# Kernel optimization log

Measured on AMD Instinct MI355X. Metric: run time of the kernel, lower is better.

## Reference

```python
import jax, jax.numpy as jnp
import numpy as np

N_NODES = 100000
N_EDGES = 1600000
IN_FEATS = 128
HIDDEN = 64
OUT_FEATS = 64
N_LABELS = 8


def setup_inputs() -> dict:
    key = jax.random.key(0)
    ks = jax.random.split(key, 10)
    glorot = lambda k, fi, fo: jax.random.normal(k, (fi, fo), jnp.float32) * jnp.sqrt(2.0 / (fi + fo))
    return {
        "features": jax.random.normal(ks[0], (N_NODES, IN_FEATS), jnp.float32),
        "edge_src": jax.random.randint(ks[1], (N_EDGES,), 0, N_NODES, jnp.int32),
        "edge_dst": jax.random.randint(ks[2], (N_EDGES,), 0, N_NODES, jnp.int32),
        "edge_types": jax.random.randint(ks[3], (N_EDGES,), 0, 4, jnp.int32),
        "W1": glorot(ks[4], IN_FEATS, HIDDEN),
        "b1": jnp.zeros((HIDDEN,), jnp.float32),
        "W2": glorot(ks[5], HIDDEN, OUT_FEATS),
        "b2": jnp.zeros((OUT_FEATS,), jnp.float32),
        "Wp": glorot(ks[6], OUT_FEATS, N_LABELS),
        "bp": jnp.zeros((N_LABELS,), jnp.float32),
    }


def _degree_norms(edge_src, edge_dst, n_nodes):
    ones = jnp.ones(edge_src.shape[0], jnp.float32)
    deg_out = jax.ops.segment_sum(ones, edge_src, num_segments=n_nodes)
    deg_in = jax.ops.segment_sum(ones, edge_dst, num_segments=n_nodes)
    # DGL clamps degrees to min 1 before pow(-0.5)
    norm_src = jnp.maximum(deg_out, 1.0) ** -0.5  # [N]
    norm_dst = jnp.maximum(deg_in, 1.0) ** -0.5   # [N]
    return norm_src, norm_dst


def _graph_conv(x, W, b, edge_src, edge_dst, norm_src, norm_dst, n_nodes):
    # norm='both': scale src, dense transform first (mult_first), aggregate, scale dst
    h = (x * norm_src[:, None]) @ W            # [N, out]
    msg = h[edge_src]                          # [E, out] gather
    agg = jax.ops.segment_sum(msg, edge_dst, num_segments=n_nodes)  # [N, out] scatter-add
    return agg * norm_dst[:, None] + b


def reference(features, edge_src, edge_dst, edge_types, W1, b1, W2, b2, Wp, bp):
    n_nodes = features.shape[0]
    norm_src, norm_dst = _degree_norms(edge_src, edge_dst, n_nodes)
    x = jax.nn.relu(_graph_conv(features, W1, b1, edge_src, edge_dst, norm_src, norm_dst, n_nodes))
    # dropout is identity in eval mode
    x = jax.nn.relu(_graph_conv(x, W2, b2, edge_src, edge_dst, norm_src, norm_dst, n_nodes))
    logits = x @ Wp + bp                       # [N, n_labels]
    return jax.nn.softmax(logits, axis=1)
```

## Files before the change

kernel.cpp:

```cpp
#include <hip/hip_runtime.h>
#include <hip/hip_fp16.h>
#include <math.h>


#define NODES   100000
#define INF     128
#define HID     64
#define NLAB    8

#define SB      512
#define NSB     ((NODES + SB - 1) / SB)
#define NHALF   ((NODES + 255) / 256)
#define SCAP    9000
#define CAPH    4600
#define PCHUNK  8192
#define PEPT    (PCHUNK / 256)
#define SRCMASK 0x1FFFF
#define GSTRIDE 16

#define WCVT_ELEMS (64 * (INF + 8) + 64 * (HID + 8))
#define WCVT_WGS   ((WCVT_ELEMS + 255) / 256)

union H8 { int4 i4; __half2 h2[4]; unsigned int u[4]; };
union H2U { __half2 h; unsigned int u; };

typedef _Float16 half8 __attribute__((ext_vector_type(8)));
typedef float floatx4 __attribute__((ext_vector_type(4)));

__device__ __forceinline__ void fma_mix2(float& a0, float& a1, unsigned int h2) {
    asm("v_fma_mix_f32 %0, %2, 1.0, %0 op_sel_hi:[1,0,0]\n\t"
        "v_fma_mix_f32 %1, %2, 1.0, %1 op_sel:[1,0,0] op_sel_hi:[1,0,0]"
        : "+v"(a0), "+v"(a1) : "v"(h2));
}


__global__ void build1_kernel(const int* __restrict__ src, const int* __restrict__ dst,
                              int* __restrict__ gcur_d, int* __restrict__ gcur_s,
                              int* __restrict__ dreg, unsigned short* __restrict__ sreg,
                              int E, int partWGs,
                              const float* __restrict__ W1, const float* __restrict__ W2,
                              _Float16* __restrict__ wt1, _Float16* __restrict__ wt2) {
    __shared__ int hd[NHALF], bd[NHALF], hs[NSB], bs[NSB];
    const int tid = threadIdx.x;

    if (blockIdx.x >= partWGs) {
        const int N1 = 64 * (INF + 8);
        const int N2 = 64 * (HID + 8);
        int i = (blockIdx.x - partWGs) * 256 + tid;
        if (i < N1) {
            int n = i / (INF + 8), k = i % (INF + 8);
            wt1[i] = (k < INF) ? (_Float16)W1[k * 64 + n] : (_Float16)0.f;
        } else if (i < N1 + N2) {
            int j = i - N1;
            int n = j / (HID + 8), k = j % (HID + 8);
            wt2[j] = (k < HID) ? (_Float16)W2[k * 64 + n] : (_Float16)0.f;
        }
        return;
    }

    const int e0 = blockIdx.x * PCHUNK;

    for (int i = tid; i < NHALF; i += 256) { hd[i] = 0; }
    for (int i = tid; i < NSB; i += 256) { hs[i] = 0; }
    __syncthreads();

    int es[PEPT], ed[PEPT];
#pragma unroll
    for (int i = 0; i < PEPT; ++i) {
        int e = e0 + tid + i * 256;
        if (e < E) {
            es[i] = src[e]; ed[i] = dst[e];
            atomicAdd(&hd[ed[i] >> 8], 1);
            atomicAdd(&hs[es[i] >> 9], 1);
        } else es[i] = -1;
    }
    __syncthreads();

    for (int b = tid; b < NHALF; b += 256) {
        int c = hd[b]; bd[b] = c ? atomicAdd(&gcur_d[b * GSTRIDE], c) : 0;
    }
    for (int b = tid; b < NSB; b += 256) {
        int c = hs[b]; bs[b] = c ? atomicAdd(&gcur_s[b * GSTRIDE], c) : 0;
    }
    __syncthreads();
    for (int b = tid; b < NHALF; b += 256) hd[b] = 0;
    for (int b = tid; b < NSB; b += 256) hs[b] = 0;
    __syncthreads();

#pragma unroll
    for (int i = 0; i < PEPT; ++i) {
        if (es[i] >= 0) {
            int s = es[i], d = ed[i];
            int kb = d >> 8;
            int pos = bd[kb] + atomicAdd(&hd[kb], 1);
            if (pos < CAPH) dreg[(size_t)kb * CAPH + pos] = ((d & 255) << 17) | s;
            int ks = s >> 9;
            int ps = bs[ks] + atomicAdd(&hs[ks], 1);
            if (ps < SCAP) sreg[(size_t)ks * SCAP + ps] = (unsigned short)(s & (SB - 1));
        }
    }
}


__global__ void shist_kernel(const unsigned short* __restrict__ sreg,
                             const int* __restrict__ gcur_s,
                             float* __restrict__ norm_s, int Nn) {
    __shared__ int hist[SB];
    const int tid = threadIdx.x;
    const int sb = blockIdx.x;
    for (int i = tid; i < SB; i += 256) hist[i] = 0;
    __syncthreads();
    const int cnt = min(gcur_s[sb * GSTRIDE], SCAP);
    const unsigned short* base = sreg + (size_t)sb * SCAP;
    for (int i = tid; i < cnt; i += 256) atomicAdd(&hist[base[i]], 1);
    __syncthreads();
    for (int t = tid; t < SB; t += 256) {
        int node = sb * SB + t;
        if (node < Nn) norm_s[node] = rsqrtf(fmaxf((float)hist[t], 1.0f));
    }
}


__global__ void build2_kernel(const int* __restrict__ dreg, const int* __restrict__ gcur_d,
                              int* __restrict__ csr, int* __restrict__ starts,
                              int* __restrict__ ends, float* __restrict__ norm_d,
                              const float* __restrict__ Xv, const float* __restrict__ norm,
                              const _Float16* __restrict__ Wt, __half* __restrict__ Hh,
                              int Nn) {
    __shared__ union SMem {
        struct CS { int hist[256]; int cur[256]; int wsum[4]; int sorted[CAPH]; } c;
        _Float16 w[64 * (INF + 8)];
    } sm;
    const int tid = threadIdx.x;

    if (blockIdx.x < NHALF) {
        const int j = blockIdx.x;
        const int cnt = min(gcur_d[j * GSTRIDE], CAPH);
        const int* reg = dreg + (size_t)j * CAPH;

        sm.c.hist[tid] = 0;
        __syncthreads();

        for (int i = tid; i < cnt; i += 256)
            atomicAdd(&sm.c.hist[(reg[i] >> 17) & 255], 1);
        __syncthreads();

        const int lane = tid & 63, wid = tid >> 6;
        int deg_n = sm.c.hist[tid];
        int v = deg_n;
#pragma unroll
        for (int off = 1; off < 64; off <<= 1) {
            int u = __shfl_up(v, off, 64);
            if (lane >= off) v += u;
        }
        if (lane == 63) sm.c.wsum[wid] = v;
        __syncthreads();
        int wadd = 0;
#pragma unroll
        for (int q = 0; q < 3; ++q) wadd += (q < wid) ? sm.c.wsum[q] : 0;
        int st = v + wadd - deg_n;

        int node = j * 256 + tid;
        if (node < Nn) {
            int gs = j * CAPH + st;
            int dcl = min(deg_n, max(CAPH - st, 0));
            starts[node] = gs;
            ends[node]   = gs + dcl;
            norm_d[node] = rsqrtf(fmaxf((float)deg_n, 1.0f));
        }
        sm.c.cur[tid] = st;
        __syncthreads();

        for (int i = tid; i < cnt; i += 256) {
            int pe = reg[i];
            int pos = atomicAdd(&sm.c.cur[(pe >> 17) & 255], 1);
            if (pos < CAPH) sm.c.sorted[pos] = pe & SRCMASK;
        }
        __syncthreads();

        for (int i = tid; i < cnt; i += 256) csr[(size_t)j * CAPH + i] = sm.c.sorted[i];
        return;
    }

    constexpr int K = INF;
    constexpr int KP = K + 8;
    const int bid = blockIdx.x - NHALF;

    constexpr int NI4 = 64 * KP * 2 / 16;
    for (int i = tid; i < NI4; i += 256)
        ((int4*)sm.w)[i] = ((const int4*)Wt)[i];
    __syncthreads();

    const int w = tid >> 6, lane = tid & 63;
    const int m16 = lane & 15, quad = lane >> 4;
    const int rowA = bid * 64 + w * 16 + m16;
    const int rowC = (rowA < Nn) ? rowA : (Nn - 1);

    floatx4 acc0 = {0.f, 0.f, 0.f, 0.f};
    floatx4 acc1 = acc0, acc2 = acc0, acc3 = acc0;

#pragma unroll
    for (int c = 0; c < K / 32; ++c) {
        const int k0 = c * 32 + quad * 8;
        const float* xrow = Xv + (size_t)rowC * K;
        float4 xa = *(const float4*)(xrow + k0);
        float4 xb = *(const float4*)(xrow + k0 + 4);
        half8 a;
        a[0] = (_Float16)xa.x; a[1] = (_Float16)xa.y;
        a[2] = (_Float16)xa.z; a[3] = (_Float16)xa.w;
        a[4] = (_Float16)xb.x; a[5] = (_Float16)xb.y;
        a[6] = (_Float16)xb.z; a[7] = (_Float16)xb.w;
        half8 b0 = *(const half8*)&sm.w[(0 * 16 + m16) * KP + k0];
        half8 b1 = *(const half8*)&sm.w[(1 * 16 + m16) * KP + k0];
        half8 b2 = *(const half8*)&sm.w[(2 * 16 + m16) * KP + k0];
        half8 b3 = *(const half8*)&sm.w[(3 * 16 + m16) * KP + k0];
        acc0 = __builtin_amdgcn_mfma_f32_16x16x32_f16(a, b0, acc0, 0, 0, 0);
        acc1 = __builtin_amdgcn_mfma_f32_16x16x32_f16(a, b1, acc1, 0, 0, 0);
        acc2 = __builtin_amdgcn_mfma_f32_16x16x32_f16(a, b2, acc2, 0, 0, 0);
        acc3 = __builtin_amdgcn_mfma_f32_16x16x32_f16(a, b3, acc3, 0, 0, 0);
    }

    const int rbase = bid * 64 + w * 16 + quad * 4;
    floatx4 accs[4] = {acc0, acc1, acc2, acc3};
#pragma unroll
    for (int i = 0; i < 4; ++i) {
        int grow = rbase + i;
        if (grow < Nn) {
            float nm = norm[grow];
            __half* o = Hh + (size_t)grow * 64 + m16;
#pragma unroll
            for (int t = 0; t < 4; ++t)
                o[16 * t] = (__half)(accs[t][i] * nm);
        } else if (grow == Nn) {
            __half* o = Hh + (size_t)grow * 64 + m16;
#pragma unroll
            for (int t = 0; t < 4; ++t)
                o[16 * t] = (__half)0.f;
        }
    }
}


template <int K, bool IN16>
__global__ void gemm_mfma_kernel(const void* __restrict__ Xv, const float* __restrict__ norm,
                                 const _Float16* __restrict__ Wt, __half* __restrict__ Hh,
                                 int M) {
    constexpr int KP = K + 8;
    __shared__ _Float16 sWt[64 * KP];

    const int tid = threadIdx.x;
    constexpr int NI4 = 64 * KP * 2 / 16;
    for (int i = tid; i < NI4; i += 256)
        ((int4*)sWt)[i] = ((const int4*)Wt)[i];
    __syncthreads();

    const int w = tid >> 6, lane = tid & 63;
    const int m16 = lane & 15, quad = lane >> 4;
    const int rowA = blockIdx.x * 64 + w * 16 + m16;
    const int rowC = (rowA < M) ? rowA : (M - 1);

    floatx4 acc0 = {0.f, 0.f, 0.f, 0.f};
    floatx4 acc1 = acc0, acc2 = acc0, acc3 = acc0;

#pragma unroll
    for (int c = 0; c < K / 32; ++c) {
        const int k0 = c * 32 + quad * 8;
        half8 a;
        if constexpr (IN16) {
            const _Float16* xrow = (const _Float16*)Xv + (size_t)rowC * K;
            a = *(const half8*)(xrow + k0);
        } else {
            const float* xrow = (const float*)Xv + (size_t)rowC * K;
            float4 xa = *(const float4*)(xrow + k0);
            float4 xb = *(const float4*)(xrow + k0 + 4);
            a[0] = (_Float16)xa.x; a[1] = (_Float16)xa.y;
            a[2] = (_Float16)xa.z; a[3] = (_Float16)xa.w;
            a[4] = (_Float16)xb.x; a[5] = (_Float16)xb.y;
            a[6] = (_Float16)xb.z; a[7] = (_Float16)xb.w;
        }
        half8 b0 = *(const half8*)&sWt[(0 * 16 + m16) * KP + k0];
        half8 b1 = *(const half8*)&sWt[(1 * 16 + m16) * KP + k0];
        half8 b2 = *(const half8*)&sWt[(2 * 16 + m16) * KP + k0];
        half8 b3 = *(const half8*)&sWt[(3 * 16 + m16) * KP + k0];
        acc0 = __builtin_amdgcn_mfma_f32_16x16x32_f16(a, b0, acc0, 0, 0, 0);
        acc1 = __builtin_amdgcn_mfma_f32_16x16x32_f16(a, b1, acc1, 0, 0, 0);
        acc2 = __builtin_amdgcn_mfma_f32_16x16x32_f16(a, b2, acc2, 0, 0, 0);
        acc3 = __builtin_amdgcn_mfma_f32_16x16x32_f16(a, b3, acc3, 0, 0, 0);
    }

    const int rbase = blockIdx.x * 64 + w * 16 + quad * 4;
    floatx4 accs[4] = {acc0, acc1, acc2, acc3};
#pragma unroll
    for (int i = 0; i < 4; ++i) {
        int grow = rbase + i;
        if (grow < M) {
            float nm = norm[grow];
            __half* o = Hh + (size_t)grow * 64 + m16;
#pragma unroll
            for (int t = 0; t < 4; ++t)
                o[16 * t] = (__half)(accs[t][i] * nm);
        } else if (grow == M) {
            __half* o = Hh + (size_t)grow * 64 + m16;
#pragma unroll
            for (int t = 0; t < 4; ++t)
                o[16 * t] = (__half)0.f;
        }
    }
}


template <bool PROJ>
__global__ void gather_kernel(const int* __restrict__ starts, const int* __restrict__ ends,
                              const int* __restrict__ csr, const __half* __restrict__ Hh,
                              const float* __restrict__ nd, const float* __restrict__ b,
                              __half* __restrict__ Xh, const float* __restrict__ Wp,
                              const float* __restrict__ bp, float* __restrict__ out,
                              int Nn) {
    __shared__ float sW[NLAB * 65];
    __shared__ float sb_[NLAB];
    const int tid = threadIdx.x;

    if constexpr (PROJ) {
        for (int i = tid; i < 64 * NLAB; i += 256) {
            int k = i >> 3, l = i & 7;
            sW[l * 65 + k] = Wp[i];
        }
        if (tid < NLAB) sb_[tid] = bp[tid];
        __syncthreads();
    }

    const int lane = tid & 63;
    const int half32 = (lane >> 5) & 1;
    const int l32 = lane & 31;
    const int g = l32 >> 3;
    const int c = lane & 7;

    int node = blockIdx.x * 8 + ((tid >> 6) << 1) + half32;
    const bool valid = node < Nn;
    const int nodeC = valid ? node : (Nn - 1);

    const int start = starts[nodeC];
    const int deg   = ends[nodeC] - start;
    const int dmax  = max(deg, __shfl_xor(deg, 32, 64));

    float acc[8] = {0.f, 0.f, 0.f, 0.f, 0.f, 0.f, 0.f, 0.f};

    for (int base = 0; base < dmax; base += 32) {
        int off = base + l32;
        int pe = (off < deg) ? csr[start + off] : Nn;
        int ecm = min(dmax - base, 32);
        int nkp = (ecm + 7) >> 3;

        for (int k = 0; k < nkp; ++k) {
            int j0 = g + 8 * k;
            int j1 = j0 + 4;
            int s0 = __shfl(pe, (lane & 32) + j0, 64);
            int s1 = __shfl(pe, (lane & 32) + j1, 64);
            H8 v0, v1;
            v0.i4 = ((const int4*)(Hh + (size_t)s0 * 64))[c];
            v1.i4 = ((const int4*)(Hh + (size_t)s1 * 64))[c];
#pragma unroll
            for (int t = 0; t < 4; ++t) {
                H2U su;
                su.h = __hadd2(v0.h2[t], v1.h2[t]);
                fma_mix2(acc[2 * t], acc[2 * t + 1], su.u);
            }
        }
    }

#pragma unroll
    for (int m = 8; m <= 16; m <<= 1) {
#pragma unroll
        for (int k = 0; k < 8; ++k)
            acc[k] += __shfl_xor(acc[k], m, 64);
    }

    if constexpr (!PROJ) {
        if (g == 0 && valid) {
            float nm = nd[node];
            float4 b0 = ((const float4*)b)[2 * c];
            float4 b1 = ((const float4*)b)[2 * c + 1];
            H8 o;
            o.h2[0] = __floats2half2_rn(fmaxf(fmaf(acc[0], nm, b0.x), 0.f),
                                        fmaxf(fmaf(acc[1], nm, b0.y), 0.f));
            o.h2[1] = __floats2half2_rn(fmaxf(fmaf(acc[2], nm, b0.z), 0.f),
                                        fmaxf(fmaf(acc[3], nm, b0.w), 0.f));
            o.h2[2] = __floats2half2_rn(fmaxf(fmaf(acc[4], nm, b1.x), 0.f),
                                        fmaxf(fmaf(acc[5], nm, b1.y), 0.f));
            o.h2[3] = __floats2half2_rn(fmaxf(fmaf(acc[6], nm, b1.z), 0.f),
                                        fmaxf(fmaf(acc[7], nm, b1.w), 0.f));
            ((int4*)(Xh + (size_t)node * 64))[c] = o.i4;
        }
    } else {
        float nm = nd[nodeC];
        float4 b0 = ((const float4*)b)[2 * c];
        float4 b1 = ((const float4*)b)[2 * c + 1];
        float xv[8];
        xv[0] = fmaxf(fmaf(acc[0], nm, b0.x), 0.f);
        xv[1] = fmaxf(fmaf(acc[1], nm, b0.y), 0.f);
        xv[2] = fmaxf(fmaf(acc[2], nm, b0.z), 0.f);
        xv[3] = fmaxf(fmaf(acc[3], nm, b0.w), 0.f);
        xv[4] = fmaxf(fmaf(acc[4], nm, b1.x), 0.f);
        xv[5] = fmaxf(fmaf(acc[5], nm, b1.y), 0.f);
        xv[6] = fmaxf(fmaf(acc[6], nm, b1.z), 0.f);
        xv[7] = fmaxf(fmaf(acc[7], nm, b1.w), 0.f);

        const int l0 = 2 * g, l1 = l0 + 1;
        float p0 = 0.f, p1 = 0.f;
#pragma unroll
        for (int j = 0; j < 8; ++j) {
            p0 = fmaf(xv[j], sW[l0 * 65 + 8 * c + j], p0);
            p1 = fmaf(xv[j], sW[l1 * 65 + 8 * c + j], p1);
        }
        p0 += __shfl_xor(p0, 1, 64); p1 += __shfl_xor(p1, 1, 64);
        p0 += __shfl_xor(p0, 2, 64); p1 += __shfl_xor(p1, 2, 64);
        p0 += __shfl_xor(p0, 4, 64); p1 += __shfl_xor(p1, 4, 64);
        p0 += sb_[l0];
        p1 += sb_[l1];
        float mx = fmaxf(p0, p1);
        mx = fmaxf(mx, __shfl_xor(mx, 8, 64));
        mx = fmaxf(mx, __shfl_xor(mx, 16, 64));
        float e0 = __expf(p0 - mx), e1 = __expf(p1 - mx);
        float s2 = e0 + e1;
        s2 += __shfl_xor(s2, 8, 64);
        s2 += __shfl_xor(s2, 16, 64);
        float inv = 1.0f / s2;
        if (c == 0 && valid) {
            float2 o = {e0 * inv, e1 * inv};
            *(float2*)(out + (size_t)node * NLAB + l0) = o;
        }
    }
}


extern "C" void kernel_launch(void* const* d_in, const int* in_sizes, int n_in,
                              void* d_out, int out_size, void* d_ws, size_t ws_size,
                              hipStream_t stream) {
    const float* features = (const float*)d_in[0];
    const int*   edge_src = (const int*)d_in[1];
    const int*   edge_dst = (const int*)d_in[2];
    const float* W1 = (const float*)d_in[4];
    const float* b1 = (const float*)d_in[5];
    const float* W2 = (const float*)d_in[6];
    const float* b2 = (const float*)d_in[7];
    const float* Wp = (const float*)d_in[8];
    const float* bp = (const float*)d_in[9];
    float* out = (float*)d_out;

    const int N = NODES;
    const int E = in_sizes[1];

    char* p = (char*)d_ws;
    int*   csr    = (int*)p;            p += sizeof(int) * (size_t)NHALF * CAPH;
    int*   starts = (int*)p;            p += sizeof(int) * N;
    int*   ends   = (int*)p;            p += sizeof(int) * N;
    float* norm_s = (float*)p;          p += sizeof(float) * N;
    float* norm_d = (float*)p;          p += sizeof(float) * N;
    int*   gcur_d = (int*)p;            p += sizeof(int) * NHALF * GSTRIDE;
    int*   gcur_s = (int*)p;            p += sizeof(int) * NSB * GSTRIDE;
    p = (char*)(((size_t)p + 255) & ~(size_t)255);
    _Float16* wt1 = (_Float16*)p;       p += sizeof(_Float16) * 64 * (INF + 8);
    _Float16* wt2 = (_Float16*)p;       p += sizeof(_Float16) * 64 * (HID + 8);
    p = (char*)(((size_t)p + 255) & ~(size_t)255);
    __half* h     = (__half*)p;         p += sizeof(__half) * ((size_t)N + 64) * 64;
    p = (char*)(((size_t)p + 255) & ~(size_t)255);
    __half* x     = (__half*)p;         p += sizeof(__half) * (size_t)N * 64;
    int*            dreg = (int*)x;
    unsigned short* sreg = (unsigned short*)((char*)x + sizeof(int) * (size_t)NHALF * CAPH);

    hipMemsetAsync(gcur_d, 0, sizeof(int) * (NHALF + NSB) * GSTRIDE, stream);

    const int partWGs = (E + PCHUNK - 1) / PCHUNK;
    build1_kernel<<<partWGs + WCVT_WGS, 256, 0, stream>>>(edge_src, edge_dst,
                                                          gcur_d, gcur_s, dreg, sreg,
                                                          E, partWGs, W1, W2, wt1, wt2);
    shist_kernel<<<NSB, 256, 0, stream>>>(sreg, gcur_s, norm_s, N);
    build2_kernel<<<NHALF + (N + 63) / 64, 256, 0, stream>>>(dreg, gcur_d, csr, starts,
                                                             ends, norm_d,
                                                             features, norm_s, wt1, h, N);

    gather_kernel<false><<<(N + 7) / 8, 256, 0, stream>>>(starts, ends, csr, h, norm_d,
                                                          b1, x, nullptr, nullptr,
                                                          nullptr, N);

    gemm_mfma_kernel<HID, true><<<(N + 63) / 64, 256, 0, stream>>>(x, norm_s, wt2, h, N);
    gather_kernel<true><<<(N + 7) / 8, 256, 0, stream>>>(starts, ends, csr, h, norm_d,
                                                         b2, nullptr, Wp, bp, out, N);
}
```

Before: 242.5 us.

## Fuse layer-1 aggregation with layer-2 MFMA GEMM via shared-memory tile

The layer-1 gather/aggregate kernel and the layer-2 dense GEMM are merged into one kernel. Each workgroup aggregates 64 nodes into an LDS tile, then multiplies that tile by W2 with MFMA and writes the pre-scaled layer-2 features. This drops a kernel launch and the global round trip of the intermediate activations. In exchange each workgroup handles 64 nodes serially with 8 iterations per wave, so there are fewer workgroups and possibly less latency hiding for the irregular gathers.

```diff
diff --git a/kernel.cpp b/kernel.cpp
--- a/kernel.cpp
+++ b/kernel.cpp
@@ -241,43 +241,98 @@
 }
 
 
-template <int K, bool IN16>
-__global__ void gemm_mfma_kernel(const void* __restrict__ Xv, const float* __restrict__ norm,
-                                 const _Float16* __restrict__ Wt, __half* __restrict__ Hh,
-                                 int M) {
+__global__ void gather_gemm_kernel(const int* __restrict__ starts, const int* __restrict__ ends,
+                                   const int* __restrict__ csr, const __half* __restrict__ Hh,
+                                   const float* __restrict__ nd, const float* __restrict__ b,
+                                   const float* __restrict__ norm, const _Float16* __restrict__ Wt,
+                                   __half* __restrict__ Xout, int Nn) {
+    constexpr int K = HID;
     constexpr int KP = K + 8;
     __shared__ _Float16 sWt[64 * KP];
+    __shared__ _Float16 xt[64 * KP];
 
     const int tid = threadIdx.x;
     constexpr int NI4 = 64 * KP * 2 / 16;
     for (int i = tid; i < NI4; i += 256)
         ((int4*)sWt)[i] = ((const int4*)Wt)[i];
-    __syncthreads();
-
-    const int w = tid >> 6, lane = tid & 63;
+
+    const int lane = tid & 63;
+    const int half32 = (lane >> 5) & 1;
+    const int l32 = lane & 31;
+    const int g = l32 >> 3;
+    const int c = lane & 7;
+    const int w = tid >> 6;
     const int m16 = lane & 15, quad = lane >> 4;
-    const int rowA = blockIdx.x * 64 + w * 16 + m16;
-    const int rowC = (rowA < M) ? rowA : (M - 1);
+
+#pragma unroll 1
+    for (int it = 0; it < 8; ++it) {
+        const int nloc = w * 16 + it * 2 + half32;
+        const int node = blockIdx.x * 64 + nloc;
+        const int nodeC = (node < Nn) ? node : (Nn - 1);
+
+        const int start = starts[nodeC];
+        const int deg   = ends[nodeC] - start;
+        const int dmax  = max(deg, __shfl_xor(deg, 32, 64));
+
+        float acc[8] = {0.f, 0.f, 0.f, 0.f, 0.f, 0.f, 0.f, 0.f};
+
+        for (int base = 0; base < dmax; base += 32) {
+            int off = base + l32;
+            int pe = (off < deg) ? csr[start + off] : Nn;
+            int ecm = min(dmax - base, 32);
+            int nkp = (ecm + 7) >> 3;
+
+            for (int k = 0; k < nkp; ++k) {
+                int j0 = g + 8 * k;
+                int j1 = j0 + 4;
+                int s0 = __shfl(pe, (lane & 32) + j0, 64);
+                int s1 = __shfl(pe, (lane & 32) + j1, 64);
+                H8 v0, v1;
+                v0.i4 = ((const int4*)(Hh + (size_t)s0 * 64))[c];
+                v1.i4 = ((const int4*)(Hh + (size_t)s1 * 64))[c];
+#pragma unroll
+                for (int t = 0; t < 4; ++t) {
+                    H2U su;
+                    su.h = __hadd2(v0.h2[t], v1.h2[t]);
+                    fma_mix2(acc[2 * t], acc[2 * t + 1], su.u);
+                }
+            }
+        }
+
+#pragma unroll
+        for (int m = 8; m <= 16; m <<= 1) {
+#pragma unroll
+            for (int k = 0; k < 8; ++k)
+                acc[k] += __shfl_xor(acc[k], m, 64);
+        }
+
+        if (g == 0) {
+            float nm = nd[nodeC];
+            float4 bb0 = ((const float4*)b)[2 * c];
+            float4 bb1 = ((const float4*)b)[2 * c + 1];
+            H8 o;
+            o.h2[0] = __floats2half2_rn(fmaxf(fmaf(acc[0], nm, bb0.x), 0.f),
+                                        fmaxf(fmaf(acc[1], nm, bb0.y), 0.f));
+            o.h2[1] = __floats2half2_rn(fmaxf(fmaf(acc[2], nm, bb0.z), 0.f),
+                                        fmaxf(fmaf(acc[3], nm, bb0.w), 0.f));
+            o.h2[2] = __floats2half2_rn(fmaxf(fmaf(acc[4], nm, bb1.x), 0.f),
+                                        fmaxf(fmaf(acc[5], nm, bb1.y), 0.f));
+            o.h2[3] = __floats2half2_rn(fmaxf(fmaf(acc[6], nm, bb1.z), 0.f),
+                                        fmaxf(fmaf(acc[7], nm, bb1.w), 0.f));
+            *(int4*)(xt + nloc * KP + c * 8) = o.i4;
+        }
+    }
+    __syncthreads();
+
+    const int rowL = w * 16 + m16;
 
     floatx4 acc0 = {0.f, 0.f, 0.f, 0.f};
     floatx4 acc1 = acc0, acc2 = acc0, acc3 = acc0;
 
 #pragma unroll
-    for (int c = 0; c < K / 32; ++c) {
-        const int k0 = c * 32 + quad * 8;
-        half8 a;
-        if constexpr (IN16) {
-            const _Float16* xrow = (const _Float16*)Xv + (size_t)rowC * K;
-            a = *(const half8*)(xrow + k0);
-        } else {
-            const float* xrow = (const float*)Xv + (size_t)rowC * K;
-            float4 xa = *(const float4*)(xrow + k0);
-            float4 xb = *(const float4*)(xrow + k0 + 4);
-            a[0] = (_Float16)xa.x; a[1] = (_Float16)xa.y;
-            a[2] = (_Float16)xa.z; a[3] = (_Float16)xa.w;
-            a[4] = (_Float16)xb.x; a[5] = (_Float16)xb.y;
-            a[6] = (_Float16)xb.z; a[7] = (_Float16)xb.w;
-        }
+    for (int cc = 0; cc < K / 32; ++cc) {
+        const int k0 = cc * 32 + quad * 8;
+        half8 a = *(const half8*)&xt[rowL * KP + k0];
         half8 b0 = *(const half8*)&sWt[(0 * 16 + m16) * KP + k0];
         half8 b1 = *(const half8*)&sWt[(1 * 16 + m16) * KP + k0];
         half8 b2 = *(const half8*)&sWt[(2 * 16 + m16) * KP + k0];
@@ -293,14 +348,14 @@
 #pragma unroll
     for (int i = 0; i < 4; ++i) {
         int grow = rbase + i;
-        if (grow < M) {
+        if (grow < Nn) {
             float nm = norm[grow];
-            __half* o = Hh + (size_t)grow * 64 + m16;
+            __half* o = Xout + (size_t)grow * 64 + m16;
 #pragma unroll
             for (int t = 0; t < 4; ++t)
                 o[16 * t] = (__half)(accs[t][i] * nm);
-        } else if (grow == M) {
-            __half* o = Hh + (size_t)grow * 64 + m16;
+        } else if (grow == Nn) {
+            __half* o = Xout + (size_t)grow * 64 + m16;
 #pragma unroll
             for (int t = 0; t < 4; ++t)
                 o[16 * t] = (__half)0.f;
@@ -309,25 +364,21 @@
 }
 
 
-template <bool PROJ>
-__global__ void gather_kernel(const int* __restrict__ starts, const int* __restrict__ ends,
-                              const int* __restrict__ csr, const __half* __restrict__ Hh,
-                              const float* __restrict__ nd, const float* __restrict__ b,
-                              __half* __restrict__ Xh, const float* __restrict__ Wp,
-                              const float* __restrict__ bp, float* __restrict__ out,
-                              int Nn) {
+__global__ void gather_proj_kernel(const int* __restrict__ starts, const int* __restrict__ ends,
+                                   const int* __restrict__ csr, const __half* __restrict__ Hh,
+                                   const float* __restrict__ nd, const float* __restrict__ b,
+                                   const float* __restrict__ Wp, const float* __restrict__ bp,
+                                   float* __restrict__ out, int Nn) {
     __shared__ float sW[NLAB * 65];
     __shared__ float sb_[NLAB];
     const int tid = threadIdx.x;
 
-    if constexpr (PROJ) {
-        for (int i = tid; i < 64 * NLAB; i += 256) {
-            int k = i >> 3, l = i & 7;
-            sW[l * 65 + k] = Wp[i];
-        }
-        if (tid < NLAB) sb_[tid] = bp[tid];
-        __syncthreads();
-    }
+    for (int i = tid; i < 64 * NLAB; i += 256) {
+        int k = i >> 3, l = i & 7;
+        sW[l * 65 + k] = Wp[i];
+    }
+    if (tid < NLAB) sb_[tid] = bp[tid];
+    __syncthreads();
 
     const int lane = tid & 63;
     const int half32 = (lane >> 5) & 1;
@@ -375,60 +426,42 @@
             acc[k] += __shfl_xor(acc[k], m, 64);
     }
 
-    if constexpr (!PROJ) {
-        if (g == 0 && valid) {
-            float nm = nd[node];
-            float4 b0 = ((const float4*)b)[2 * c];
-            float4 b1 = ((const float4*)b)[2 * c + 1];
-            H8 o;
-            o.h2[0] = __floats2half2_rn(fmaxf(fmaf(acc[0], nm, b0.x), 0.f),
-                                        fmaxf(fmaf(acc[1], nm, b0.y), 0.f));
-            o.h2[1] = __floats2half2_rn(fmaxf(fmaf(acc[2], nm, b0.z), 0.f),
-                                        fmaxf(fmaf(acc[3], nm, b0.w), 0.f));
-            o.h2[2] = __floats2half2_rn(fmaxf(fmaf(acc[4], nm, b1.x), 0.f),
-                                        fmaxf(fmaf(acc[5], nm, b1.y), 0.f));
-            o.h2[3] = __floats2half2_rn(fmaxf(fmaf(acc[6], nm, b1.z), 0.f),
-                                        fmaxf(fmaf(acc[7], nm, b1.w), 0.f));
-            ((int4*)(Xh + (size_t)node * 64))[c] = o.i4;
-        }
-    } else {
-        float nm = nd[nodeC];
-        float4 b0 = ((const float4*)b)[2 * c];
-        float4 b1 = ((const float4*)b)[2 * c + 1];
-        float xv[8];
-        xv[0] = fmaxf(fmaf(acc[0], nm, b0.x), 0.f);
-        xv[1] = fmaxf(fmaf(acc[1], nm, b0.y), 0.f);
-        xv[2] = fmaxf(fmaf(acc[2], nm, b0.z), 0.f);
-        xv[3] = fmaxf(fmaf(acc[3], nm, b0.w), 0.f);
-        xv[4] = fmaxf(fmaf(acc[4], nm, b1.x), 0.f);
-        xv[5] = fmaxf(fmaf(acc[5], nm, b1.y), 0.f);
-        xv[6] = fmaxf(fmaf(acc[6], nm, b1.z), 0.f);
-        xv[7] = fmaxf(fmaf(acc[7], nm, b1.w), 0.f);
-
-        const int l0 = 2 * g, l1 = l0 + 1;
-        float p0 = 0.f, p1 = 0.f;
-#pragma unroll
-        for (int j = 0; j < 8; ++j) {
-            p0 = fmaf(xv[j], sW[l0 * 65 + 8 * c + j], p0);
-            p1 = fmaf(xv[j], sW[l1 * 65 + 8 * c + j], p1);
-        }
-        p0 += __shfl_xor(p0, 1, 64); p1 += __shfl_xor(p1, 1, 64);
-        p0 += __shfl_xor(p0, 2, 64); p1 += __shfl_xor(p1, 2, 64);
-        p0 += __shfl_xor(p0, 4, 64); p1 += __shfl_xor(p1, 4, 64);
-        p0 += sb_[l0];
-        p1 += sb_[l1];
-        float mx = fmaxf(p0, p1);
-        mx = fmaxf(mx, __shfl_xor(mx, 8, 64));
-        mx = fmaxf(mx, __shfl_xor(mx, 16, 64));
-        float e0 = __expf(p0 - mx), e1 = __expf(p1 - mx);
-        float s2 = e0 + e1;
-        s2 += __shfl_xor(s2, 8, 64);
-        s2 += __shfl_xor(s2, 16, 64);
-        float inv = 1.0f / s2;
-        if (c == 0 && valid) {
-            float2 o = {e0 * inv, e1 * inv};
-            *(float2*)(out + (size_t)node * NLAB + l0) = o;
-        }
+    float nm = nd[nodeC];
+    float4 b0 = ((const float4*)b)[2 * c];
+    float4 b1 = ((const float4*)b)[2 * c + 1];
+    float xv[8];
+    xv[0] = fmaxf(fmaf(acc[0], nm, b0.x), 0.f);
+    xv[1] = fmaxf(fmaf(acc[1], nm, b0.y), 0.f);
+    xv[2] = fmaxf(fmaf(acc[2], nm, b0.z), 0.f);
+    xv[3] = fmaxf(fmaf(acc[3], nm, b0.w), 0.f);
+    xv[4] = fmaxf(fmaf(acc[4], nm, b1.x), 0.f);
+    xv[5] = fmaxf(fmaf(acc[5], nm, b1.y), 0.f);
+    xv[6] = fmaxf(fmaf(acc[6], nm, b1.z), 0.f);
+    xv[7] = fmaxf(fmaf(acc[7], nm, b1.w), 0.f);
+
+    const int l0 = 2 * g, l1 = l0 + 1;
+    float p0 = 0.f, p1 = 0.f;
+#pragma unroll
+    for (int j = 0; j < 8; ++j) {
+        p0 = fmaf(xv[j], sW[l0 * 65 + 8 * c + j], p0);
+        p1 = fmaf(xv[j], sW[l1 * 65 + 8 * c + j], p1);
+    }
+    p0 += __shfl_xor(p0, 1, 64); p1 += __shfl_xor(p1, 1, 64);
+    p0 += __shfl_xor(p0, 2, 64); p1 += __shfl_xor(p1, 2, 64);
+    p0 += __shfl_xor(p0, 4, 64); p1 += __shfl_xor(p1, 4, 64);
+    p0 += sb_[l0];
+    p1 += sb_[l1];
+    float mx = fmaxf(p0, p1);
+    mx = fmaxf(mx, __shfl_xor(mx, 8, 64));
+    mx = fmaxf(mx, __shfl_xor(mx, 16, 64));
+    float e0 = __expf(p0 - mx), e1 = __expf(p1 - mx);
+    float s2 = e0 + e1;
+    s2 += __shfl_xor(s2, 8, 64);
+    s2 += __shfl_xor(s2, 16, 64);
+    float inv = 1.0f / s2;
+    if (c == 0 && valid) {
+        float2 o = {e0 * inv, e1 * inv};
+        *(float2*)(out + (size_t)node * NLAB + l0) = o;
     }
 }
 
@@ -464,7 +497,7 @@
     p = (char*)(((size_t)p + 255) & ~(size_t)255);
     __half* h     = (__half*)p;         p += sizeof(__half) * ((size_t)N + 64) * 64;
     p = (char*)(((size_t)p + 255) & ~(size_t)255);
-    __half* x     = (__half*)p;         p += sizeof(__half) * (size_t)N * 64;
+    __half* x     = (__half*)p;         p += sizeof(__half) * ((size_t)N + 64) * 64;
     int*            dreg = (int*)x;
     unsigned short* sreg = (unsigned short*)((char*)x + sizeof(int) * (size_t)NHALF * CAPH);
 
@@ -479,11 +512,9 @@
                                                              ends, norm_d,
                                                              features, norm_s, wt1, h, N);
 
-    gather_kernel<false><<<(N + 7) / 8, 256, 0, stream>>>(starts, ends, csr, h, norm_d,
-                                                          b1, x, nullptr, nullptr,
-                                                          nullptr, N);
-
-    gemm_mfma_kernel<HID, true><<<(N + 63) / 64, 256, 0, stream>>>(x, norm_s, wt2, h, N);
-    gather_kernel<true><<<(N + 7) / 8, 256, 0, stream>>>(starts, ends, csr, h, norm_d,
-                                                         b2, nullptr, Wp, bp, out, N);
-}
+    gather_gemm_kernel<<<(N + 63) / 64, 256, 0, stream>>>(starts, ends, csr, h, norm_d,
+                                                          b1, norm_s, wt2, x, N);
+
+    gather_proj_kernel<<<(N + 7) / 8, 256, 0, stream>>>(starts, ends, csr, x, norm_d,
+                                                        b2, Wp, bp, out, N);
+}
```

New measurement: 232.9 us. 1.04x faster.
